# Optimization experiments

Hardware: AMD Instinct MI355X
Metric: run time of the kernel (lower is better)

Reference implementation:

```python
import jax, jax.numpy as jnp
import numpy as np

B, T, D = 32, 4096, 512  # D = 2 * hidden_size


def setup_inputs() -> dict:
    key = jax.random.key(0)
    k_h, k_w1, k_b1, k_w2 = jax.random.split(key, 4)
    scale = 1.0 / np.sqrt(D)
    return {
        "hidden_states": jax.random.normal(k_h, (B, T, D), dtype=jnp.float32),
        "W1": jax.random.normal(k_w1, (D, D), dtype=jnp.float32) * scale,
        "b1": jax.random.normal(k_b1, (D,), dtype=jnp.float32) * scale,
        "W2": jax.random.normal(k_w2, (D, D), dtype=jnp.float32) * scale,
    }


def reference(hidden_states, W1, b1, W2):
    # u = tanh(h @ W1^T + b1)        [B, T, D]
    u = jnp.tanh(jnp.einsum("btd,ed->bte", hidden_states, W1) + b1)
    # alphas = softmax over time axis of u @ W2^T (no bias)   [B, T, D]
    alphas = jax.nn.softmax(jnp.einsum("btd,ed->bte", u, W2), axis=1)
    # Original loop cats weighted [T, D] slices along dim 0 then sums dim 0,
    # i.e. a global reduction over batch AND time -> [D]
    return jnp.sum(hidden_states * alphas, axis=(0, 1))
```

## Files before the change

kernel.cpp:

```cpp
#include <hip/hip_runtime.h>
#include <math.h>

#define BATCH 32
#define TLEN  4096
#define DDIM  512
#define BM    64
#define BLOCK 512

typedef __attribute__((ext_vector_type(8)))  short bf16x8;
typedef __attribute__((ext_vector_type(16))) float f32x16;
typedef __attribute__((ext_vector_type(4)))  short s16x4;

__device__ __forceinline__ short f32_to_bf16_rne(float f) {
    union { float f; unsigned int u; } v; v.f = f;
    unsigned int r = (v.u + 0x7FFFu + ((v.u >> 16) & 1u)) >> 16;
    return (short)r;
}
__device__ __forceinline__ float fast_tanh(float x) {
    x = fminf(fmaxf(x, -15.f), 15.f);
    float t = __expf(2.0f * x);
    return (t - 1.0f) / (t + 1.0f);
}

__device__ __forceinline__ int lds_idx(int r, int c) {
    int g = (c >> 3) ^ (r & 31);
    return r * DDIM + (g << 3) + (c & 7);
}

__global__ void prep_kernel(const float* __restrict__ W1, const float* __restrict__ W2,
                            short* __restrict__ W1pk, short* __restrict__ W2pk,
                            float* __restrict__ lbuf, float* __restrict__ gbuf) {
    int i = blockIdx.x * blockDim.x + threadIdx.x;
    int e  = i >> 6;
    int d0 = (i & 63) << 3;
    int E = e >> 5, r = e & 31, C = d0 >> 4, half = (d0 >> 3) & 1;
    size_t src = (size_t)e * DDIM + d0;
    size_t dst = ((size_t)(E * 32 + C) * 64 + half * 32 + r) * 8;
    bf16x8 p1, p2;
    #pragma unroll
    for (int j = 0; j < 8; ++j) {
        p1[j] = f32_to_bf16_rne(W1[src + j]);
        p2[j] = f32_to_bf16_rne(W2[src + j]);
    }
    *(bf16x8*)&W1pk[dst] = p1;
    *(bf16x8*)&W2pk[dst] = p2;
    if (i < BATCH * DDIM) { lbuf[i] = 0.f; gbuf[i] = 0.f; }
}

__global__ __launch_bounds__(BLOCK, 2)
void main_kernel(const float* __restrict__ h,
                 const short* __restrict__ W1pk,
                 const float* __restrict__ b1,
                 const short* __restrict__ W2pk,
                 float* __restrict__ lbuf, float* __restrict__ gbuf) {
    __shared__ __align__(16) short sh[BM * DDIM];

    const int tid  = threadIdx.x;
    const int row0 = blockIdx.x * BM;
    const int b    = row0 / TLEN;

    {
        const float4* hp = (const float4*)(h + (size_t)row0 * DDIM);
        #pragma unroll
        for (int i = 0; i < (BM * DDIM / 4) / BLOCK; ++i) {
            int idx  = tid + i * BLOCK;
            float4 v = hp[idx];
            int flat = idx * 4;
            int r = flat >> 9;
            int c = flat & (DDIM - 1);
            s16x4 p;
            p.x = f32_to_bf16_rne(v.x); p.y = f32_to_bf16_rne(v.y);
            p.z = f32_to_bf16_rne(v.z); p.w = f32_to_bf16_rne(v.w);
            *(s16x4*)&sh[lds_idx(r, c)] = p;
        }
    }
    __syncthreads();

    const int wave = tid >> 6;
    const int lane = tid & 63;
    const int l32  = lane & 31;
    const int h5   = lane >> 5;
    const int e0   = wave * 64;

    f32x16 acc[2][2];
    #pragma unroll
    for (int i = 0; i < 2; ++i)
        #pragma unroll
        for (int j = 0; j < 2; ++j)
            #pragma unroll
            for (int r = 0; r < 16; ++r) acc[i][j][r] = 0.f;

    const short* W1p = W1pk + (size_t)(e0 >> 5) * (32 * 512) + lane * 8;
    bf16x8 wc[2][2], wn[2][2];
    #pragma unroll
    for (int eb = 0; eb < 2; ++eb)
        #pragma unroll
        for (int ks = 0; ks < 2; ++ks)
            wc[eb][ks] = *(const bf16x8*)(W1p + (eb * 32 + ks) * 512);

    for (int k0 = 0; k0 < DDIM; k0 += 32) {
        const int kb = k0 >> 4;
        bf16x8 hf[2][2];
        #pragma unroll
        for (int tb = 0; tb < 2; ++tb)
            #pragma unroll
            for (int ks = 0; ks < 2; ++ks)
                hf[tb][ks] = *(const bf16x8*)&sh[lds_idx(tb * 32 + l32,
                                                         k0 + ks * 16 + 8 * h5)];
        #pragma unroll
        for (int eb = 0; eb < 2; ++eb)
            #pragma unroll
            for (int ks = 0; ks < 2; ++ks)
                wn[eb][ks] = *(const bf16x8*)(W1p + (eb * 32 + kb + 2 + ks) * 512);
        #pragma unroll
        for (int eb = 0; eb < 2; ++eb)
            #pragma unroll
            for (int tb = 0; tb < 2; ++tb)
                #pragma unroll
                for (int ks = 0; ks < 2; ++ks)
                    acc[eb][tb] = __builtin_amdgcn_mfma_f32_32x32x16_bf16(
                        wc[eb][ks], hf[tb][ks], acc[eb][tb], 0, 0, 0);
        #pragma unroll
        for (int eb = 0; eb < 2; ++eb)
            #pragma unroll
            for (int ks = 0; ks < 2; ++ks) wc[eb][ks] = wn[eb][ks];
    }

    const short* W2p = W2pk + (size_t)(e0 >> 5) * (32 * 512) + lane * 8;
    bf16x8 w2c[2][2], w2n[2][2];
    #pragma unroll
    for (int cb = 0; cb < 2; ++cb)
        #pragma unroll
        for (int ks = 0; ks < 2; ++ks)
            w2c[cb][ks] = *(const bf16x8*)(W2p + (cb * 32 + ks) * 512);

    #pragma unroll
    for (int eb = 0; eb < 2; ++eb) {
        float4 bv[4];
        #pragma unroll
        for (int q = 0; q < 4; ++q)
            bv[q] = *(const float4*)&b1[e0 + 32 * eb + 4 * h5 + 8 * q];
        #pragma unroll
        for (int tb = 0; tb < 2; ++tb)
            #pragma unroll
            for (int r = 0; r < 16; ++r)
                acc[eb][tb][r] = fast_tanh(acc[eb][tb][r] + bv[r >> 2][r & 3]);
    }

    __syncthreads();

    #pragma unroll
    for (int eb = 0; eb < 2; ++eb)
        #pragma unroll
        for (int tb = 0; tb < 2; ++tb) {
            int t = tb * 32 + l32;
            #pragma unroll
            for (int q = 0; q < 4; ++q) {
                int e = e0 + 32 * eb + 4 * h5 + 8 * q;
                s16x4 p;
                p.x = f32_to_bf16_rne(acc[eb][tb][4 * q + 0]);
                p.y = f32_to_bf16_rne(acc[eb][tb][4 * q + 1]);
                p.z = f32_to_bf16_rne(acc[eb][tb][4 * q + 2]);
                p.w = f32_to_bf16_rne(acc[eb][tb][4 * q + 3]);
                *(s16x4*)&sh[lds_idx(t, e)] = p;
            }
        }
    __syncthreads();

    f32x16 acc2[2][2];
    #pragma unroll
    for (int i = 0; i < 2; ++i)
        #pragma unroll
        for (int j = 0; j < 2; ++j)
            #pragma unroll
            for (int r = 0; r < 16; ++r) acc2[i][j][r] = 0.f;

    for (int k0 = 0; k0 < DDIM; k0 += 32) {
        const int kb = k0 >> 4;
        bf16x8 uf[2][2];
        #pragma unroll
        for (int tb = 0; tb < 2; ++tb)
            #pragma unroll
            for (int ks = 0; ks < 2; ++ks)
                uf[tb][ks] = *(const bf16x8*)&sh[lds_idx(tb * 32 + l32,
                                                         k0 + ks * 16 + 8 * h5)];
        #pragma unroll
        for (int cb = 0; cb < 2; ++cb)
            #pragma unroll
            for (int ks = 0; ks < 2; ++ks)
                w2n[cb][ks] = *(const bf16x8*)(W2p + (cb * 32 + kb + 2 + ks) * 512);
        #pragma unroll
        for (int tb = 0; tb < 2; ++tb)
            #pragma unroll
            for (int cb = 0; cb < 2; ++cb)
                #pragma unroll
                for (int ks = 0; ks < 2; ++ks)
                    acc2[tb][cb] = __builtin_amdgcn_mfma_f32_32x32x16_bf16(
                        uf[tb][ks], w2c[cb][ks], acc2[tb][cb], 0, 0, 0);
        #pragma unroll
        for (int cb = 0; cb < 2; ++cb)
            #pragma unroll
            for (int ks = 0; ks < 2; ++ks) w2c[cb][ks] = w2n[cb][ks];
    }

    #pragma unroll
    for (int cb = 0; cb < 2; ++cb) {
        const int e2 = e0 + 32 * cb + l32;
        const float* hp2 = h + (size_t)row0 * DDIM + e2;
        float lsum = 0.f, gsum = 0.f;
        #pragma unroll
        for (int tb = 0; tb < 2; ++tb)
            #pragma unroll
            for (int r = 0; r < 16; ++r) {
                int t = tb * 32 + 4 * h5 + (r & 3) + 8 * (r >> 2);
                float ev = __expf(acc2[tb][cb][r]);
                lsum += ev;
                gsum += ev * hp2[(size_t)t * DDIM];
            }
        lsum += __shfl_xor(lsum, 32);
        gsum += __shfl_xor(gsum, 32);
        if (h5 == 0) {
            atomicAdd(&lbuf[b * DDIM + e2], lsum);
            atomicAdd(&gbuf[b * DDIM + e2], gsum);
        }
    }
}

__global__ void finish_kernel(const float* __restrict__ lbuf,
                              const float* __restrict__ gbuf,
                              float* __restrict__ out) {
    int d = blockIdx.x * blockDim.x + threadIdx.x;
    float s = 0.f;
    #pragma unroll
    for (int b = 0; b < BATCH; ++b)
        s += gbuf[b * DDIM + d] / lbuf[b * DDIM + d];
    out[d] = s;
}

extern "C" void kernel_launch(void* const* d_in, const int* in_sizes, int n_in,
                              void* d_out, int out_size, void* d_ws, size_t ws_size,
                              hipStream_t stream) {
    const float* h  = (const float*)d_in[0];
    const float* W1 = (const float*)d_in[1];
    const float* b1 = (const float*)d_in[2];
    const float* W2 = (const float*)d_in[3];
    float* out = (float*)d_out;

    char* ws = (char*)d_ws;
    short* W1pk = (short*)ws;
    short* W2pk = (short*)(ws + 512 * 1024);
    float* lbuf = (float*)(ws + 1024 * 1024);
    float* gbuf = (float*)(ws + 1024 * 1024 + 64 * 1024);

    prep_kernel<<<128, 256, 0, stream>>>(W1, W2, W1pk, W2pk, lbuf, gbuf);
    main_kernel<<<(BATCH * TLEN) / BM, BLOCK, 0, stream>>>(h, W1pk, b1, W2pk, lbuf, gbuf);
    finish_kernel<<<2, 256, 0, stream>>>(lbuf, gbuf, out);
}
```

Baseline: 537.2 us.

## Process multiple row tiles per block with register-staged prefetch of next tile

Each block now loops over eight 64-row tiles instead of one, cutting the grid from 2048 to 256 blocks. The h slice for the next tile is loaded into registers during the tanh/GEMM2 phase and written to LDS after GEMM2, so global latency overlaps compute. The 16 float4 staging registers per thread raise register pressure, and the smaller grid may leave CUs underused on a 256-CU part. Per-tile atomics are unchanged.

```diff
diff --git a/kernel.cpp b/kernel.cpp
--- a/kernel.cpp
+++ b/kernel.cpp
@@ -6,6 +6,7 @@
 #define DDIM  512
 #define BM    64
 #define BLOCK 512
+#define NT    8
 
 typedef __attribute__((ext_vector_type(8)))  short bf16x8;
 typedef __attribute__((ext_vector_type(16))) float f32x16;
@@ -56,13 +57,21 @@
     __shared__ __align__(16) short sh[BM * DDIM];
 
     const int tid  = threadIdx.x;
-    const int row0 = blockIdx.x * BM;
-    const int b    = row0 / TLEN;
+    const int wave = tid >> 6;
+    const int lane = tid & 63;
+    const int l32  = lane & 31;
+    const int h5   = lane >> 5;
+    const int e0   = wave * 64;
+    const int tile0 = blockIdx.x * NT;
+    const int b     = (tile0 * BM) / TLEN;
+
+    const short* W1p = W1pk + (size_t)(e0 >> 5) * (32 * 512) + lane * 8;
+    const short* W2p = W2pk + (size_t)(e0 >> 5) * (32 * 512) + lane * 8;
 
     {
-        const float4* hp = (const float4*)(h + (size_t)row0 * DDIM);
-        #pragma unroll
-        for (int i = 0; i < (BM * DDIM / 4) / BLOCK; ++i) {
+        const float4* hp = (const float4*)(h + (size_t)tile0 * BM * DDIM);
+        #pragma unroll
+        for (int i = 0; i < 16; ++i) {
             int idx  = tid + i * BLOCK;
             float4 v = hp[idx];
             int flat = idx * 4;
@@ -74,154 +83,174 @@
             *(s16x4*)&sh[lds_idx(r, c)] = p;
         }
     }
-    __syncthreads();
-
-    const int wave = tid >> 6;
-    const int lane = tid & 63;
-    const int l32  = lane & 31;
-    const int h5   = lane >> 5;
-    const int e0   = wave * 64;
-
-    f32x16 acc[2][2];
-    #pragma unroll
-    for (int i = 0; i < 2; ++i)
-        #pragma unroll
-        for (int j = 0; j < 2; ++j)
-            #pragma unroll
-            for (int r = 0; r < 16; ++r) acc[i][j][r] = 0.f;
-
-    const short* W1p = W1pk + (size_t)(e0 >> 5) * (32 * 512) + lane * 8;
-    bf16x8 wc[2][2], wn[2][2];
-    #pragma unroll
-    for (int eb = 0; eb < 2; ++eb)
-        #pragma unroll
-        for (int ks = 0; ks < 2; ++ks)
-            wc[eb][ks] = *(const bf16x8*)(W1p + (eb * 32 + ks) * 512);
-
-    for (int k0 = 0; k0 < DDIM; k0 += 32) {
-        const int kb = k0 >> 4;
-        bf16x8 hf[2][2];
-        #pragma unroll
-        for (int tb = 0; tb < 2; ++tb)
+
+    for (int t = 0; t < NT; ++t) {
+        const int row0 = (tile0 + t) * BM;
+        __syncthreads();
+
+        f32x16 acc[2][2];
+        #pragma unroll
+        for (int i = 0; i < 2; ++i)
+            #pragma unroll
+            for (int j = 0; j < 2; ++j)
+                #pragma unroll
+                for (int r = 0; r < 16; ++r) acc[i][j][r] = 0.f;
+
+        bf16x8 wc[2][2], wn[2][2];
+        #pragma unroll
+        for (int eb = 0; eb < 2; ++eb)
             #pragma unroll
             for (int ks = 0; ks < 2; ++ks)
-                hf[tb][ks] = *(const bf16x8*)&sh[lds_idx(tb * 32 + l32,
-                                                         k0 + ks * 16 + 8 * h5)];
+                wc[eb][ks] = *(const bf16x8*)(W1p + (eb * 32 + ks) * 512);
+
+        for (int k0 = 0; k0 < DDIM; k0 += 32) {
+            const int kb = k0 >> 4;
+            bf16x8 hf[2][2];
+            #pragma unroll
+            for (int tb = 0; tb < 2; ++tb)
+                #pragma unroll
+                for (int ks = 0; ks < 2; ++ks)
+                    hf[tb][ks] = *(const bf16x8*)&sh[lds_idx(tb * 32 + l32,
+                                                             k0 + ks * 16 + 8 * h5)];
+            #pragma unroll
+            for (int eb = 0; eb < 2; ++eb)
+                #pragma unroll
+                for (int ks = 0; ks < 2; ++ks)
+                    wn[eb][ks] = *(const bf16x8*)(W1p + (eb * 32 + kb + 2 + ks) * 512);
+            #pragma unroll
+            for (int eb = 0; eb < 2; ++eb)
+                #pragma unroll
+                for (int tb = 0; tb < 2; ++tb)
+                    #pragma unroll
+                    for (int ks = 0; ks < 2; ++ks)
+                        acc[eb][tb] = __builtin_amdgcn_mfma_f32_32x32x16_bf16(
+                            wc[eb][ks], hf[tb][ks], acc[eb][tb], 0, 0, 0);
+            #pragma unroll
+            for (int eb = 0; eb < 2; ++eb)
+                #pragma unroll
+                for (int ks = 0; ks < 2; ++ks) wc[eb][ks] = wn[eb][ks];
+        }
+
+        bf16x8 w2c[2][2], w2n[2][2];
+        #pragma unroll
+        for (int cb = 0; cb < 2; ++cb)
+            #pragma unroll
+            for (int ks = 0; ks < 2; ++ks)
+                w2c[cb][ks] = *(const bf16x8*)(W2p + (cb * 32 + ks) * 512);
+
+        #pragma unroll
+        for (int eb = 0; eb < 2; ++eb) {
+            float4 bv[4];
+            #pragma unroll
+            for (int q = 0; q < 4; ++q)
+                bv[q] = *(const float4*)&b1[e0 + 32 * eb + 4 * h5 + 8 * q];
+            #pragma unroll
+            for (int tb = 0; tb < 2; ++tb)
+                #pragma unroll
+                for (int r = 0; r < 16; ++r)
+                    acc[eb][tb][r] = fast_tanh(acc[eb][tb][r] + bv[r >> 2][r & 3]);
+        }
+
+        __syncthreads();
+
+        float4 stg[16];
+        const bool pf = (t + 1 < NT);
+        if (pf) {
+            const float4* hpn = (const float4*)(h + (size_t)(row0 + BM) * DDIM);
+            #pragma unroll
+            for (int i = 0; i < 16; ++i) stg[i] = hpn[tid + i * BLOCK];
+        }
+
         #pragma unroll
         for (int eb = 0; eb < 2; ++eb)
             #pragma unroll
-            for (int ks = 0; ks < 2; ++ks)
-                wn[eb][ks] = *(const bf16x8*)(W1p + (eb * 32 + kb + 2 + ks) * 512);
-        #pragma unroll
-        for (int eb = 0; eb < 2; ++eb)
-            #pragma unroll
-            for (int tb = 0; tb < 2; ++tb)
-                #pragma unroll
-                for (int ks = 0; ks < 2; ++ks)
-                    acc[eb][tb] = __builtin_amdgcn_mfma_f32_32x32x16_bf16(
-                        wc[eb][ks], hf[tb][ks], acc[eb][tb], 0, 0, 0);
-        #pragma unroll
-        for (int eb = 0; eb < 2; ++eb)
-            #pragma unroll
-            for (int ks = 0; ks < 2; ++ks) wc[eb][ks] = wn[eb][ks];
-    }
-
-    const short* W2p = W2pk + (size_t)(e0 >> 5) * (32 * 512) + lane * 8;
-    bf16x8 w2c[2][2], w2n[2][2];
-    #pragma unroll
-    for (int cb = 0; cb < 2; ++cb)
-        #pragma unroll
-        for (int ks = 0; ks < 2; ++ks)
-            w2c[cb][ks] = *(const bf16x8*)(W2p + (cb * 32 + ks) * 512);
-
-    #pragma unroll
-    for (int eb = 0; eb < 2; ++eb) {
-        float4 bv[4];
-        #pragma unroll
-        for (int q = 0; q < 4; ++q)
-            bv[q] = *(const float4*)&b1[e0 + 32 * eb + 4 * h5 + 8 * q];
-        #pragma unroll
-        for (int tb = 0; tb < 2; ++tb)
-            #pragma unroll
-            for (int r = 0; r < 16; ++r)
-                acc[eb][tb][r] = fast_tanh(acc[eb][tb][r] + bv[r >> 2][r & 3]);
-    }
-
-    __syncthreads();
-
-    #pragma unroll
-    for (int eb = 0; eb < 2; ++eb)
-        #pragma unroll
-        for (int tb = 0; tb < 2; ++tb) {
-            int t = tb * 32 + l32;
-            #pragma unroll
-            for (int q = 0; q < 4; ++q) {
-                int e = e0 + 32 * eb + 4 * h5 + 8 * q;
+            for (int tb = 0; tb < 2; ++tb) {
+                int tt = tb * 32 + l32;
+                #pragma unroll
+                for (int q = 0; q < 4; ++q) {
+                    int e = e0 + 32 * eb + 4 * h5 + 8 * q;
+                    s16x4 p;
+                    p.x = f32_to_bf16_rne(acc[eb][tb][4 * q + 0]);
+                    p.y = f32_to_bf16_rne(acc[eb][tb][4 * q + 1]);
+                    p.z = f32_to_bf16_rne(acc[eb][tb][4 * q + 2]);
+                    p.w = f32_to_bf16_rne(acc[eb][tb][4 * q + 3]);
+                    *(s16x4*)&sh[lds_idx(tt, e)] = p;
+                }
+            }
+        __syncthreads();
+
+        f32x16 acc2[2][2];
+        #pragma unroll
+        for (int i = 0; i < 2; ++i)
+            #pragma unroll
+            for (int j = 0; j < 2; ++j)
+                #pragma unroll
+                for (int r = 0; r < 16; ++r) acc2[i][j][r] = 0.f;
+
+        for (int k0 = 0; k0 < DDIM; k0 += 32) {
+            const int kb = k0 >> 4;
+            bf16x8 uf[2][2];
+            #pragma unroll
+            for (int tb = 0; tb < 2; ++tb)
+                #pragma unroll
+                for (int ks = 0; ks < 2; ++ks)
+                    uf[tb][ks] = *(const bf16x8*)&sh[lds_idx(tb * 32 + l32,
+                                                             k0 + ks * 16 + 8 * h5)];
+            #pragma unroll
+            for (int cb = 0; cb < 2; ++cb)
+                #pragma unroll
+                for (int ks = 0; ks < 2; ++ks)
+                    w2n[cb][ks] = *(const bf16x8*)(W2p + (cb * 32 + kb + 2 + ks) * 512);
+            #pragma unroll
+            for (int tb = 0; tb < 2; ++tb)
+                #pragma unroll
+                for (int cb = 0; cb < 2; ++cb)
+                    #pragma unroll
+                    for (int ks = 0; ks < 2; ++ks)
+                        acc2[tb][cb] = __builtin_amdgcn_mfma_f32_32x32x16_bf16(
+                            uf[tb][ks], w2c[cb][ks], acc2[tb][cb], 0, 0, 0);
+            #pragma unroll
+            for (int cb = 0; cb < 2; ++cb)
+                #pragma unroll
+                for (int ks = 0; ks < 2; ++ks) w2c[cb][ks] = w2n[cb][ks];
+        }
+
+        __syncthreads();
+
+        if (pf) {
+            #pragma unroll
+            for (int i = 0; i < 16; ++i) {
+                int idx  = tid + i * BLOCK;
+                int flat = idx * 4;
+                int r = flat >> 9;
+                int c = flat & (DDIM - 1);
                 s16x4 p;
-                p.x = f32_to_bf16_rne(acc[eb][tb][4 * q + 0]);
-                p.y = f32_to_bf16_rne(acc[eb][tb][4 * q + 1]);
-                p.z = f32_to_bf16_rne(acc[eb][tb][4 * q + 2]);
-                p.w = f32_to_bf16_rne(acc[eb][tb][4 * q + 3]);
-                *(s16x4*)&sh[lds_idx(t, e)] = p;
+                p.x = f32_to_bf16_rne(stg[i].x); p.y = f32_to_bf16_rne(stg[i].y);
+                p.z = f32_to_bf16_rne(stg[i].z); p.w = f32_to_bf16_rne(stg[i].w);
+                *(s16x4*)&sh[lds_idx(r, c)] = p;
             }
         }
-    __syncthreads();
-
-    f32x16 acc2[2][2];
-    #pragma unroll
-    for (int i = 0; i < 2; ++i)
-        #pragma unroll
-        for (int j = 0; j < 2; ++j)
-            #pragma unroll
-            for (int r = 0; r < 16; ++r) acc2[i][j][r] = 0.f;
-
-    for (int k0 = 0; k0 < DDIM; k0 += 32) {
-        const int kb = k0 >> 4;
-        bf16x8 uf[2][2];
-        #pragma unroll
-        for (int tb = 0; tb < 2; ++tb)
-            #pragma unroll
-            for (int ks = 0; ks < 2; ++ks)
-                uf[tb][ks] = *(const bf16x8*)&sh[lds_idx(tb * 32 + l32,
-                                                         k0 + ks * 16 + 8 * h5)];
-        #pragma unroll
-        for (int cb = 0; cb < 2; ++cb)
-            #pragma unroll
-            for (int ks = 0; ks < 2; ++ks)
-                w2n[cb][ks] = *(const bf16x8*)(W2p + (cb * 32 + kb + 2 + ks) * 512);
-        #pragma unroll
-        for (int tb = 0; tb < 2; ++tb)
-            #pragma unroll
-            for (int cb = 0; cb < 2; ++cb)
-                #pragma unroll
-                for (int ks = 0; ks < 2; ++ks)
-                    acc2[tb][cb] = __builtin_amdgcn_mfma_f32_32x32x16_bf16(
-                        uf[tb][ks], w2c[cb][ks], acc2[tb][cb], 0, 0, 0);
-        #pragma unroll
-        for (int cb = 0; cb < 2; ++cb)
-            #pragma unroll
-            for (int ks = 0; ks < 2; ++ks) w2c[cb][ks] = w2n[cb][ks];
-    }
-
-    #pragma unroll
-    for (int cb = 0; cb < 2; ++cb) {
-        const int e2 = e0 + 32 * cb + l32;
-        const float* hp2 = h + (size_t)row0 * DDIM + e2;
-        float lsum = 0.f, gsum = 0.f;
-        #pragma unroll
-        for (int tb = 0; tb < 2; ++tb)
-            #pragma unroll
-            for (int r = 0; r < 16; ++r) {
-                int t = tb * 32 + 4 * h5 + (r & 3) + 8 * (r >> 2);
-                float ev = __expf(acc2[tb][cb][r]);
-                lsum += ev;
-                gsum += ev * hp2[(size_t)t * DDIM];
+
+        #pragma unroll
+        for (int cb = 0; cb < 2; ++cb) {
+            const int e2 = e0 + 32 * cb + l32;
+            const float* hp2 = h + (size_t)row0 * DDIM + e2;
+            float lsum = 0.f, gsum = 0.f;
+            #pragma unroll
+            for (int tb = 0; tb < 2; ++tb)
+                #pragma unroll
+                for (int r = 0; r < 16; ++r) {
+                    int tt = tb * 32 + 4 * h5 + (r & 3) + 8 * (r >> 2);
+                    float ev = __expf(acc2[tb][cb][r]);
+                    lsum += ev;
+                    gsum += ev * hp2[(size_t)tt * DDIM];
+                }
+            lsum += __shfl_xor(lsum, 32);
+            gsum += __shfl_xor(gsum, 32);
+            if (h5 == 0) {
+                atomicAdd(&lbuf[b * DDIM + e2], lsum);
+                atomicAdd(&gbuf[b * DDIM + e2], gsum);
             }
-        lsum += __shfl_xor(lsum, 32);
-        gsum += __shfl_xor(gsum, 32);
-        if (h5 == 0) {
-            atomicAdd(&lbuf[b * DDIM + e2], lsum);
-            atomicAdd(&gbuf[b * DDIM + e2], gsum);
         }
     }
 }
@@ -253,6 +282,6 @@
     float* gbuf = (float*)(ws + 1024 * 1024 + 64 * 1024);
 
     prep_kernel<<<128, 256, 0, stream>>>(W1, W2, W1pk, W2pk, lbuf, gbuf);
-    main_kernel<<<(BATCH * TLEN) / BM, BLOCK, 0, stream>>>(h, W1pk, b1, W2pk, lbuf, gbuf);
+    main_kernel<<<(BATCH * TLEN) / (BM * NT), BLOCK, 0, stream>>>(h, W1pk, b1, W2pk, lbuf, gbuf);
     finish_kernel<<<2, 256, 0, stream>>>(lbuf, gbuf, out);
 }
```

After: 1.070 ms. 1.99x slower.

## Halve row tile, raise occupancy, and reuse bf16 h from LDS in epilogue

Applied to the files above, without the earlier changes.

Cuts the per-block row tile from 64 to 32, halving the accumulator register footprint, and raises launch bounds to allow four blocks per CU. The final weighted sum now reads h values from the bf16 tile already in LDS, which are stashed in registers before u overwrites the buffer, instead of re-reading fp32 h from global memory. This removes a second strided global read of h and should improve latency hiding. The trade-off is twice as many blocks, each reloading W1/W2 fragments with half the reuse, twice as many atomics, and the use of bf16-rounded h in the final product, which lowers accuracy.

```diff
diff --git a/kernel.cpp b/kernel.cpp
--- a/kernel.cpp
+++ b/kernel.cpp
@@ -4,7 +4,7 @@
 #define BATCH 32
 #define TLEN  4096
 #define DDIM  512
-#define BM    64
+#define BM    32
 #define BLOCK 512
 
 typedef __attribute__((ext_vector_type(8)))  short bf16x8;
@@ -15,6 +15,11 @@
     union { float f; unsigned int u; } v; v.f = f;
     unsigned int r = (v.u + 0x7FFFu + ((v.u >> 16) & 1u)) >> 16;
     return (short)r;
+}
+__device__ __forceinline__ float bf16_to_f32(unsigned int s) {
+    union { unsigned int u; float f; } v;
+    v.u = (s & 0xFFFFu) << 16;
+    return v.f;
 }
 __device__ __forceinline__ float fast_tanh(float x) {
     x = fminf(fmaxf(x, -15.f), 15.f);
@@ -47,7 +52,7 @@
     if (i < BATCH * DDIM) { lbuf[i] = 0.f; gbuf[i] = 0.f; }
 }
 
-__global__ __launch_bounds__(BLOCK, 2)
+__global__ __launch_bounds__(BLOCK, 4)
 void main_kernel(const float* __restrict__ h,
                  const short* __restrict__ W1pk,
                  const float* __restrict__ b1,
@@ -82,13 +87,11 @@
     const int h5   = lane >> 5;
     const int e0   = wave * 64;
 
-    f32x16 acc[2][2];
+    f32x16 acc[2];
     #pragma unroll
     for (int i = 0; i < 2; ++i)
         #pragma unroll
-        for (int j = 0; j < 2; ++j)
-            #pragma unroll
-            for (int r = 0; r < 16; ++r) acc[i][j][r] = 0.f;
+        for (int r = 0; r < 16; ++r) acc[i][r] = 0.f;
 
     const short* W1p = W1pk + (size_t)(e0 >> 5) * (32 * 512) + lane * 8;
     bf16x8 wc[2][2], wn[2][2];
@@ -100,13 +103,10 @@
 
     for (int k0 = 0; k0 < DDIM; k0 += 32) {
         const int kb = k0 >> 4;
-        bf16x8 hf[2][2];
-        #pragma unroll
-        for (int tb = 0; tb < 2; ++tb)
-            #pragma unroll
-            for (int ks = 0; ks < 2; ++ks)
-                hf[tb][ks] = *(const bf16x8*)&sh[lds_idx(tb * 32 + l32,
-                                                         k0 + ks * 16 + 8 * h5)];
+        bf16x8 hf[2];
+        #pragma unroll
+        for (int ks = 0; ks < 2; ++ks)
+            hf[ks] = *(const bf16x8*)&sh[lds_idx(l32, k0 + ks * 16 + 8 * h5)];
         #pragma unroll
         for (int eb = 0; eb < 2; ++eb)
             #pragma unroll
@@ -115,11 +115,9 @@
         #pragma unroll
         for (int eb = 0; eb < 2; ++eb)
             #pragma unroll
-            for (int tb = 0; tb < 2; ++tb)
-                #pragma unroll
-                for (int ks = 0; ks < 2; ++ks)
-                    acc[eb][tb] = __builtin_amdgcn_mfma_f32_32x32x16_bf16(
-                        wc[eb][ks], hf[tb][ks], acc[eb][tb], 0, 0, 0);
+            for (int ks = 0; ks < 2; ++ks)
+                acc[eb] = __builtin_amdgcn_mfma_f32_32x32x16_bf16(
+                    wc[eb][ks], hf[ks], acc[eb], 0, 0, 0);
         #pragma unroll
         for (int eb = 0; eb < 2; ++eb)
             #pragma unroll
@@ -141,62 +139,63 @@
         for (int q = 0; q < 4; ++q)
             bv[q] = *(const float4*)&b1[e0 + 32 * eb + 4 * h5 + 8 * q];
         #pragma unroll
-        for (int tb = 0; tb < 2; ++tb)
-            #pragma unroll
-            for (int r = 0; r < 16; ++r)
-                acc[eb][tb][r] = fast_tanh(acc[eb][tb][r] + bv[r >> 2][r & 3]);
+        for (int r = 0; r < 16; ++r)
+            acc[eb][r] = fast_tanh(acc[eb][r] + bv[r >> 2][r & 3]);
+    }
+
+    unsigned int hpk[2][8];
+    #pragma unroll
+    for (int cb = 0; cb < 2; ++cb) {
+        int e2 = e0 + 32 * cb + l32;
+        #pragma unroll
+        for (int q = 0; q < 8; ++q) {
+            int tt0 = 4 * h5 + ((2 * q) & 3) + 8 * (q >> 1);
+            unsigned int lo = (unsigned short)sh[lds_idx(tt0, e2)];
+            unsigned int hi = (unsigned short)sh[lds_idx(tt0 + 1, e2)];
+            hpk[cb][q] = lo | (hi << 16);
+        }
     }
 
     __syncthreads();
 
     #pragma unroll
-    for (int eb = 0; eb < 2; ++eb)
-        #pragma unroll
-        for (int tb = 0; tb < 2; ++tb) {
-            int t = tb * 32 + l32;
-            #pragma unroll
-            for (int q = 0; q < 4; ++q) {
-                int e = e0 + 32 * eb + 4 * h5 + 8 * q;
-                s16x4 p;
-                p.x = f32_to_bf16_rne(acc[eb][tb][4 * q + 0]);
-                p.y = f32_to_bf16_rne(acc[eb][tb][4 * q + 1]);
-                p.z = f32_to_bf16_rne(acc[eb][tb][4 * q + 2]);
-                p.w = f32_to_bf16_rne(acc[eb][tb][4 * q + 3]);
-                *(s16x4*)&sh[lds_idx(t, e)] = p;
-            }
-        }
+    for (int eb = 0; eb < 2; ++eb) {
+        #pragma unroll
+        for (int q = 0; q < 4; ++q) {
+            int e = e0 + 32 * eb + 4 * h5 + 8 * q;
+            s16x4 p;
+            p.x = f32_to_bf16_rne(acc[eb][4 * q + 0]);
+            p.y = f32_to_bf16_rne(acc[eb][4 * q + 1]);
+            p.z = f32_to_bf16_rne(acc[eb][4 * q + 2]);
+            p.w = f32_to_bf16_rne(acc[eb][4 * q + 3]);
+            *(s16x4*)&sh[lds_idx(l32, e)] = p;
+        }
+    }
     __syncthreads();
 
-    f32x16 acc2[2][2];
+    f32x16 acc2[2];
     #pragma unroll
     for (int i = 0; i < 2; ++i)
         #pragma unroll
-        for (int j = 0; j < 2; ++j)
-            #pragma unroll
-            for (int r = 0; r < 16; ++r) acc2[i][j][r] = 0.f;
+        for (int r = 0; r < 16; ++r) acc2[i][r] = 0.f;
 
     for (int k0 = 0; k0 < DDIM; k0 += 32) {
         const int kb = k0 >> 4;
-        bf16x8 uf[2][2];
-        #pragma unroll
-        for (int tb = 0; tb < 2; ++tb)
-            #pragma unroll
-            for (int ks = 0; ks < 2; ++ks)
-                uf[tb][ks] = *(const bf16x8*)&sh[lds_idx(tb * 32 + l32,
-                                                         k0 + ks * 16 + 8 * h5)];
+        bf16x8 uf[2];
+        #pragma unroll
+        for (int ks = 0; ks < 2; ++ks)
+            uf[ks] = *(const bf16x8*)&sh[lds_idx(l32, k0 + ks * 16 + 8 * h5)];
         #pragma unroll
         for (int cb = 0; cb < 2; ++cb)
             #pragma unroll
             for (int ks = 0; ks < 2; ++ks)
                 w2n[cb][ks] = *(const bf16x8*)(W2p + (cb * 32 + kb + 2 + ks) * 512);
         #pragma unroll
-        for (int tb = 0; tb < 2; ++tb)
-            #pragma unroll
-            for (int cb = 0; cb < 2; ++cb)
-                #pragma unroll
-                for (int ks = 0; ks < 2; ++ks)
-                    acc2[tb][cb] = __builtin_amdgcn_mfma_f32_32x32x16_bf16(
-                        uf[tb][ks], w2c[cb][ks], acc2[tb][cb], 0, 0, 0);
+        for (int cb = 0; cb < 2; ++cb)
+            #pragma unroll
+            for (int ks = 0; ks < 2; ++ks)
+                acc2[cb] = __builtin_amdgcn_mfma_f32_32x32x16_bf16(
+                    uf[ks], w2c[cb][ks], acc2[cb], 0, 0, 0);
         #pragma unroll
         for (int cb = 0; cb < 2; ++cb)
             #pragma unroll
@@ -206,17 +205,14 @@
     #pragma unroll
     for (int cb = 0; cb < 2; ++cb) {
         const int e2 = e0 + 32 * cb + l32;
-        const float* hp2 = h + (size_t)row0 * DDIM + e2;
         float lsum = 0.f, gsum = 0.f;
         #pragma unroll
-        for (int tb = 0; tb < 2; ++tb)
-            #pragma unroll
-            for (int r = 0; r < 16; ++r) {
-                int t = tb * 32 + 4 * h5 + (r & 3) + 8 * (r >> 2);
-                float ev = __expf(acc2[tb][cb][r]);
-                lsum += ev;
-                gsum += ev * hp2[(size_t)t * DDIM];
-            }
+        for (int r = 0; r < 16; ++r) {
+            float hv = bf16_to_f32(hpk[cb][r >> 1] >> (16 * (r & 1)));
+            float ev = __expf(acc2[cb][r]);
+            lsum += ev;
+            gsum += ev * hv;
+        }
         lsum += __shfl_xor(lsum, 32);
         gsum += __shfl_xor(gsum, 32);
         if (h5 == 0) {
```

New measurement: 536.0 us. Within noise of the previous version (-0.2%).
